# Optimization experiments

Hardware: AMD Instinct MI355X
Metric: run time of the kernel (lower is better)

The kernel has to match this reference:

```python
import jax, jax.numpy as jnp
import numpy as np

N = 50000
E = 800000
IN_CH = 128
HID = 128
HEADS = 2
NUM_GRAPHS = 1024
NEG_SLOPE = 0.2  # PyG GATConv default


def _gat_conv(x, src, dst, n, W, a_src, a_dst, b, heads, out_ch, concat):
    # x: [N, F_in]; src/dst: [E'] (self-loops already included)
    h = (x @ W).reshape(n, heads, out_ch)                # [N, H, C]
    alpha_src = jnp.sum(h * a_src, axis=-1)              # [N, H]
    alpha_dst = jnp.sum(h * a_dst, axis=-1)              # [N, H]
    e = alpha_src[src] + alpha_dst[dst]                  # [E', H]
    e = jnp.where(e > 0, e, NEG_SLOPE * e)               # leaky_relu
    # softmax over incoming edges of each destination node
    emax = jax.ops.segment_max(e, dst, num_segments=n)   # [N, H]
    ex = jnp.exp(e - emax[dst])
    denom = jax.ops.segment_sum(ex, dst, num_segments=n)
    alpha = ex / denom[dst]                              # [E', H]
    msg = h[src] * alpha[:, :, None]                     # [E', H, C]
    out = jax.ops.segment_sum(msg, dst, num_segments=n)  # [N, H, C]
    if concat:
        out = out.reshape(n, heads * out_ch)
    else:
        out = out.mean(axis=1)
    return out + b


def setup_inputs() -> dict:
    key = jax.random.key(0)
    ks = jax.random.split(key, 16)
    x = jax.random.normal(ks[0], (N, IN_CH), dtype=jnp.float32)
    edge_index = jax.random.randint(ks[1], (2, E), 0, N, dtype=jnp.int64)
    batch = jnp.sort(jax.random.randint(ks[2], (N,), 0, NUM_GRAPHS, dtype=jnp.int64))
    s = lambda fan_in: 1.0 / np.sqrt(fan_in)
    W1 = jax.random.normal(ks[3], (IN_CH, HEADS * HID), dtype=jnp.float32) * s(IN_CH)
    att_src1 = jax.random.normal(ks[4], (HEADS, HID), dtype=jnp.float32) * s(HID)
    att_dst1 = jax.random.normal(ks[5], (HEADS, HID), dtype=jnp.float32) * s(HID)
    b1 = jnp.zeros((HEADS * HID,), dtype=jnp.float32)
    W2 = jax.random.normal(ks[6], (HEADS * HID, HID), dtype=jnp.float32) * s(HEADS * HID)
    att_src2 = jax.random.normal(ks[7], (1, HID), dtype=jnp.float32) * s(HID)
    att_dst2 = jax.random.normal(ks[8], (1, HID), dtype=jnp.float32) * s(HID)
    b2 = jnp.zeros((HID,), dtype=jnp.float32)
    lw1 = jax.random.normal(ks[9], (HID, HID // 2), dtype=jnp.float32) * s(HID)
    lb1 = jnp.zeros((HID // 2,), dtype=jnp.float32)
    lw2 = jax.random.normal(ks[10], (HID // 2, 1), dtype=jnp.float32) * s(HID // 2)
    lb2 = jnp.zeros((1,), dtype=jnp.float32)
    return {"x": x, "edge_index": edge_index, "batch": batch, "num_graphs": NUM_GRAPHS,
            "W1": W1, "att_src1": att_src1, "att_dst1": att_dst1, "b1": b1,
            "W2": W2, "att_src2": att_src2, "att_dst2": att_dst2, "b2": b2,
            "lw1": lw1, "lb1": lb1, "lw2": lw2, "lb2": lb2}


def reference(x, edge_index, batch, num_graphs, W1, att_src1, att_dst1, b1, W2, att_src2, att_dst2, b2, lw1, lb1, lw2, lb2):
    n = x.shape[0]
    # PyG GATConv adds self-loops by default
    loops = jnp.arange(n, dtype=edge_index.dtype)
    src = jnp.concatenate([edge_index[0], loops])
    dst = jnp.concatenate([edge_index[1], loops])
    h = jax.nn.relu(_gat_conv(x, src, dst, n, W1, att_src1, att_dst1, b1, HEADS, HID, concat=True))
    h = jax.nn.relu(_gat_conv(h, src, dst, n, W2, att_src2, att_dst2, b2, 1, HID, concat=True))
    # global mean pool over batch index
    sums = jax.ops.segment_sum(h, batch, num_segments=num_graphs)        # [G, HID]
    cnt = jax.ops.segment_sum(jnp.ones((n,), h.dtype), batch, num_segments=num_graphs)
    pooled = sums / jnp.maximum(cnt, 1.0)[:, None]
    z = jax.nn.relu(pooled @ lw1 + lb1)
    return z @ lw2 + lb2                                                 # [G, 1]
```

## Files before the change

### kernel.cpp

```cpp
#include <hip/hip_runtime.h>

#define NN 50000
#define NE 800000
#define NEP (NN + NE)
#define NG 1024

__device__ inline unsigned short f2b(float f) {
    unsigned int u = __float_as_uint(f);
    unsigned int r = (u + 0x7FFFu + ((u >> 16) & 1u)) >> 16;
    return (unsigned short)r;
}
__device__ inline float b2f(unsigned short b) {
    return __uint_as_float(((unsigned int)b) << 16);
}

__global__ void detect_i64(const int* __restrict__ raw, int n32, int* __restrict__ flag)
{
    __shared__ int nz;
    int tid = threadIdx.x;
    if (tid == 0) nz = 0;
    __syncthreads();
    int cnt = 0;
    for (int i = tid; i < 1024; i += 256) {
        int p = n32 - 2048 + 2 * i + 1;
        if (p >= 0 && p < n32 && raw[p] != 0) cnt++;
    }
    atomicAdd(&nz, cnt);
    __syncthreads();
    if (tid == 0) flag[0] = (nz == 0) ? 1 : 0;
}

__global__ void cvt_idx(const int* __restrict__ raw, const int* __restrict__ flag,
                        int* __restrict__ out, int n)
{
    int i = blockIdx.x * 256 + threadIdx.x;
    if (i >= n) return;
    out[i] = flag[0] ? raw[2 * i] : raw[i];
}

__global__ void edge_hist(const int* __restrict__ ei, int* __restrict__ cnt)
{
    int e = blockIdx.x * 256 + threadIdx.x;
    if (e >= NEP) return;
    int dst = (e < NE) ? ei[NE + e] : (e - NE);
    atomicAdd(&cnt[dst], 1);
}

__global__ __launch_bounds__(1024) void scan_counts(const int* __restrict__ cnt,
                                                    int* __restrict__ rowptr, int n)
{
    __shared__ int wsums[16];
    __shared__ int carry_s;
    int tid = threadIdx.x, lane = tid & 63, wid = tid >> 6;
    if (tid == 0) carry_s = 0;
    __syncthreads();
    for (int base = 0; base < n; base += 1024) {
        int i = base + tid;
        int v = (i < n) ? cnt[i] : 0;
        int s = v;
        #pragma unroll
        for (int off = 1; off < 64; off <<= 1) {
            int t = __shfl_up(s, off);
            if (lane >= off) s += t;
        }
        if (lane == 63) wsums[wid] = s;
        __syncthreads();
        if (wid == 0 && lane < 16) {
            int ws = wsums[lane];
            #pragma unroll
            for (int off = 1; off < 16; off <<= 1) {
                int t = __shfl_up(ws, off);
                if (lane >= off) ws += t;
            }
            wsums[lane] = ws;
        }
        __syncthreads();
        int wave_off = (wid == 0) ? 0 : wsums[wid - 1];
        int carry = carry_s;
        if (i < n) rowptr[i] = carry + wave_off + s - v;
        int total = wsums[15];
        __syncthreads();
        if (tid == 0) carry_s = carry + total;
        __syncthreads();
    }
    if (tid == 0) rowptr[n] = carry_s;
}

__global__ void copy_int(const int* __restrict__ a, int* __restrict__ b, int n)
{
    int i = blockIdx.x * 256 + threadIdx.x;
    if (i < n) b[i] = a[i];
}

__global__ void edge_scatter(const int* __restrict__ ei, int* __restrict__ cursor,
                             int* __restrict__ csr_src)
{
    int e = blockIdx.x * 256 + threadIdx.x;
    if (e >= NEP) return;
    int src, dst;
    if (e < NE) { src = ei[e]; dst = ei[NE + e]; }
    else        { src = dst = e - NE; }
    int pos = atomicAdd(&cursor[dst], 1);
    csr_src[pos] = src;
}

template <int HEADS>
__global__ __launch_bounds__(256) void gemm_fused(const float* __restrict__ A,
                                                  const float* __restrict__ B,
                                                  unsigned short* __restrict__ Cb,
                                                  const float* __restrict__ att_src,
                                                  const float* __restrict__ att_dst,
                                                  float* __restrict__ asrc,
                                                  float* __restrict__ adst,
                                                  int M, int N, int K)
{
    const int BM = 128, BN = 128, BK = 16;
    __shared__ float As[BK][BM];
    __shared__ float Bs[BK][BN];
    int tid = threadIdx.x;
    int tx = tid & 15, ty = tid >> 4;
    int row0 = blockIdx.x * BM, col0 = blockIdx.y * BN;
    float acc[8][8] = {};
    for (int k0 = 0; k0 < K; k0 += BK) {
        #pragma unroll
        for (int i = 0; i < 2; i++) {
            int f4 = tid + i * 256;
            int r  = f4 >> 2;
            int c4 = (f4 & 3) << 2;
            float4 v = make_float4(0.f, 0.f, 0.f, 0.f);
            int gr = row0 + r;
            if (gr < M) v = *(const float4*)&A[(size_t)gr * K + k0 + c4];
            As[c4 + 0][r] = v.x; As[c4 + 1][r] = v.y;
            As[c4 + 2][r] = v.z; As[c4 + 3][r] = v.w;
        }
        #pragma unroll
        for (int i = 0; i < 2; i++) {
            int f4 = tid + i * 256;
            int r  = f4 >> 5;
            int c4 = (f4 & 31) << 2;
            *(float4*)&Bs[r][c4] = *(const float4*)&B[(size_t)(k0 + r) * N + col0 + c4];
        }
        __syncthreads();
        #pragma unroll
        for (int k = 0; k < BK; k++) {
            float av[8], bv[8];
            *(float4*)&av[0] = *(const float4*)&As[k][ty * 8];
            *(float4*)&av[4] = *(const float4*)&As[k][ty * 8 + 4];
            *(float4*)&bv[0] = *(const float4*)&Bs[k][tx * 8];
            *(float4*)&bv[4] = *(const float4*)&Bs[k][tx * 8 + 4];
            #pragma unroll
            for (int i = 0; i < 8; i++)
                #pragma unroll
                for (int j = 0; j < 8; j++)
                    acc[i][j] += av[i] * bv[j];
        }
        __syncthreads();
    }

    float vs[8], vd[8];
    #pragma unroll
    for (int j = 0; j < 8; j++) {
        vs[j] = att_src[col0 + tx * 8 + j];
        vd[j] = att_dst[col0 + tx * 8 + j];
    }
    int head = col0 >> 7;
    #pragma unroll
    for (int i = 0; i < 8; i++) {
        int gr = row0 + ty * 8 + i;
        if (gr < M) {
            float ps = 0.f, pd = 0.f;
            #pragma unroll
            for (int j = 0; j < 8; j++) { ps += acc[i][j] * vs[j]; pd += acc[i][j] * vd[j]; }
            #pragma unroll
            for (int off = 8; off > 0; off >>= 1) {
                ps += __shfl_xor(ps, off);
                pd += __shfl_xor(pd, off);
            }
            if (tx == 0) {
                atomicAdd(&asrc[gr * HEADS + head], ps);
                atomicAdd(&adst[gr * HEADS + head], pd);
            }
            #pragma unroll
            for (int j = 0; j < 8; j += 4) {
                ushort4 bvv;
                bvv.x = f2b(acc[i][j + 0]); bvv.y = f2b(acc[i][j + 1]);
                bvv.z = f2b(acc[i][j + 2]); bvv.w = f2b(acc[i][j + 3]);
                *(ushort4*)&Cb[(size_t)gr * N + col0 + tx * 8 + j] = bvv;
            }
        }
    }
}

template <int HEADS>
__global__ __launch_bounds__(256) void gat_aggregate(const unsigned short* __restrict__ hb,
                                                     const float* __restrict__ asrc,
                                                     const float* __restrict__ adst,
                                                     const int* __restrict__ rowptr,
                                                     const int* __restrict__ csr_src,
                                                     const float* __restrict__ bias,
                                                     float* __restrict__ out, int n)
{
    const int CH   = HEADS * 128;
    const int PER  = CH / 64;
    const int MAXE = 128;
    __shared__ float w_lds[4][MAXE * HEADS];
    __shared__ int   s_lds[4][MAXE];
    int wid = threadIdx.x >> 6, lane = threadIdx.x & 63;
    int node = blockIdx.x * 4 + wid;
    if (node >= n) return;

    int start = rowptr[node], end = rowptr[node + 1];
    int deg = end - start;
    bool fast = (deg <= MAXE);
    int head = (PER == 4) ? (lane >> 5) : 0;

    float ad[HEADS], m[HEADS], dsum[HEADS];
    #pragma unroll
    for (int hh = 0; hh < HEADS; hh++) { ad[hh] = adst[node * HEADS + hh]; m[hh] = -1e30f; dsum[hh] = 0.f; }

    for (int base = 0; base < deg; base += 64) {
        int j = base + lane;
        if (j < deg) {
            int s = csr_src[start + j];
            if (fast) s_lds[wid][j] = s;
            #pragma unroll
            for (int hh = 0; hh < HEADS; hh++) {
                float v = asrc[s * HEADS + hh] + ad[hh];
                v = (v > 0.f) ? v : 0.2f * v;
                if (fast) w_lds[wid][j * HEADS + hh] = v;
                m[hh] = fmaxf(m[hh], v);
            }
        }
    }
    #pragma unroll
    for (int hh = 0; hh < HEADS; hh++)
        #pragma unroll
        for (int off = 32; off > 0; off >>= 1)
            m[hh] = fmaxf(m[hh], __shfl_xor(m[hh], off));

    for (int base = 0; base < deg; base += 64) {
        int j = base + lane;
        if (j < deg) {
            #pragma unroll
            for (int hh = 0; hh < HEADS; hh++) {
                float v;
                if (fast) v = w_lds[wid][j * HEADS + hh];
                else {
                    int s = csr_src[start + j];
                    v = asrc[s * HEADS + hh] + ad[hh];
                    v = (v > 0.f) ? v : 0.2f * v;
                }
                float ex = __expf(v - m[hh]);
                if (fast) w_lds[wid][j * HEADS + hh] = ex;
                dsum[hh] += ex;
            }
        }
    }
    #pragma unroll
    for (int hh = 0; hh < HEADS; hh++)
        #pragma unroll
        for (int off = 32; off > 0; off >>= 1)
            dsum[hh] += __shfl_xor(dsum[hh], off);

    float m_l    = (HEADS == 2 && head) ? m[HEADS - 1] : m[0];
    float ad_l   = (HEADS == 2 && head) ? ad[HEADS - 1] : ad[0];
    float inv_l  = 1.0f / ((HEADS == 2 && head) ? dsum[HEADS - 1] : dsum[0]);

    float acc[PER];
    #pragma unroll
    for (int p = 0; p < PER; p++) acc[p] = 0.f;

    auto edge_sw = [&](int j, int& s, float& wgt) {
        if (fast) {
            s   = s_lds[wid][j];
            wgt = w_lds[wid][j * HEADS + head] * inv_l;
        } else {
            s = csr_src[start + j];
            float v = asrc[s * HEADS + head] + ad_l;
            v = (v > 0.f) ? v : 0.2f * v;
            wgt = __expf(v - m_l) * inv_l;
        }
    };

    const int U = 8;
    int j = 0;
    for (; j + U <= deg; j += U) {
        int su[U]; float wu[U];
        #pragma unroll
        for (int u = 0; u < U; u++) edge_sw(j + u, su[u], wu[u]);
        if (PER == 4) {
            ushort4 hv[U];
            #pragma unroll
            for (int u = 0; u < U; u++)
                hv[u] = *(const ushort4*)&hb[(size_t)su[u] * CH + lane * 4];
            #pragma unroll
            for (int u = 0; u < U; u++) {
                acc[0] += wu[u] * b2f(hv[u].x); acc[1] += wu[u] * b2f(hv[u].y);
                acc[2] += wu[u] * b2f(hv[u].z); acc[3] += wu[u] * b2f(hv[u].w);
            }
        } else {
            ushort2 hv[U];
            #pragma unroll
            for (int u = 0; u < U; u++)
                hv[u] = *(const ushort2*)&hb[(size_t)su[u] * CH + lane * 2];
            #pragma unroll
            for (int u = 0; u < U; u++) {
                acc[0] += wu[u] * b2f(hv[u].x); acc[1] += wu[u] * b2f(hv[u].y);
            }
        }
    }
    for (; j < deg; j++) {
        int s; float wgt;
        edge_sw(j, s, wgt);
        if (PER == 4) {
            ushort4 hv = *(const ushort4*)&hb[(size_t)s * CH + lane * 4];
            acc[0] += wgt * b2f(hv.x); acc[1] += wgt * b2f(hv.y);
            acc[2] += wgt * b2f(hv.z); acc[3] += wgt * b2f(hv.w);
        } else {
            ushort2 hv = *(const ushort2*)&hb[(size_t)s * CH + lane * 2];
            acc[0] += wgt * b2f(hv.x); acc[1] += wgt * b2f(hv.y);
        }
    }

    #pragma unroll
    for (int p = 0; p < PER; p++) {
        float v = acc[p] + bias[lane * PER + p];
        out[(size_t)node * CH + lane * PER + p] = fmaxf(v, 0.f);
    }
}

__global__ void find_bounds(const int* __restrict__ batch, int* __restrict__ bstart)
{
    int g = blockIdx.x * 256 + threadIdx.x;
    if (g > NG) return;
    if (g == NG) { bstart[NG] = NN; return; }
    int lo = 0, hi = NN;
    while (lo < hi) { int mid = (lo + hi) >> 1; if (batch[mid] < g) lo = mid + 1; else hi = mid; }
    bstart[g] = lo;
}

__global__ __launch_bounds__(256) void pool_seg(const float* __restrict__ h,
                                                const int* __restrict__ bstart,
                                                float* __restrict__ pooled)
{
    __shared__ float2 part[4][64];
    int g = blockIdx.x;
    int start = bstart[g], end = bstart[g + 1];
    int lane = threadIdx.x & 63, w = threadIdx.x >> 6;
    float2 acc = make_float2(0.f, 0.f);
    for (int i = start + w; i < end; i += 4) {
        float2 v = *(const float2*)&h[(size_t)i * 128 + lane * 2];
        acc.x += v.x; acc.y += v.y;
    }
    part[w][lane] = acc;
    __syncthreads();
    if (w == 0) {
        float2 s = part[0][lane];
        s.x += part[1][lane].x + part[2][lane].x + part[3][lane].x;
        s.y += part[1][lane].y + part[2][lane].y + part[3][lane].y;
        float invc = 1.0f / fmaxf((float)(end - start), 1.0f);
        pooled[g * 128 + lane * 2 + 0] = s.x * invc;
        pooled[g * 128 + lane * 2 + 1] = s.y * invc;
    }
}

__global__ __launch_bounds__(64) void head_mlp(const float* __restrict__ pooled,
                                               const float* __restrict__ lw1,
                                               const float* __restrict__ lb1,
                                               const float* __restrict__ lw2,
                                               const float* __restrict__ lb2,
                                               float* __restrict__ out)
{
    int g = blockIdx.x, lane = threadIdx.x;
    __shared__ float p[128];
    p[lane]      = pooled[g * 128 + lane];
    p[lane + 64] = pooled[g * 128 + lane + 64];
    __syncthreads();
    float z = lb1[lane];
    #pragma unroll 8
    for (int k = 0; k < 128; k++) z += p[k] * lw1[k * 64 + lane];
    z = fmaxf(z, 0.f);
    float v = z * lw2[lane];
    #pragma unroll
    for (int off = 32; off > 0; off >>= 1) v += __shfl_xor(v, off);
    if (lane == 0) out[g] = v + lb2[0];
}

extern "C" void kernel_launch(void* const* d_in, const int* in_sizes, int n_in,
                              void* d_out, int out_size, void* d_ws, size_t ws_size,
                              hipStream_t stream)
{
    const float* x      = (const float*)d_in[0];
    const int*   ei_raw = (const int*)d_in[1];
    const int*   bat_raw= (const int*)d_in[2];
    const float* W1   = (const float*)d_in[4];
    const float* as1  = (const float*)d_in[5];
    const float* ad1  = (const float*)d_in[6];
    const float* b1   = (const float*)d_in[7];
    const float* W2   = (const float*)d_in[8];
    const float* as2  = (const float*)d_in[9];
    const float* ad2  = (const float*)d_in[10];
    const float* b2   = (const float*)d_in[11];
    const float* lw1  = (const float*)d_in[12];
    const float* lb1  = (const float*)d_in[13];
    const float* lw2  = (const float*)d_in[14];
    const float* lb2  = (const float*)d_in[15];
    float* out = (float*)d_out;

    char* w = (char*)d_ws;
    auto alloc = [&](size_t bytes) { char* p = w; w += (bytes + 255) & ~size_t(255); return p; };
    float*          o1    = (float*)alloc((size_t)NN * 256 * 4);
    float*          o2    = (float*)alloc((size_t)NN * 128 * 4);
    unsigned short* h1b   = (unsigned short*)alloc((size_t)NN * 256 * 2);
    unsigned short* h2b   = (unsigned short*)alloc((size_t)NN * 128 * 2);
    float* alph  = (float*)alloc((size_t)NN * 6 * 4);
    float* asrc1 = alph;
    float* adst1 = alph + (size_t)NN * 2;
    float* asrc2 = alph + (size_t)NN * 4;
    float* adst2 = alph + (size_t)NN * 5;
    int*   cnts  = (int*)alloc((size_t)NN * 4);
    int*   rowp  = (int*)alloc((size_t)(NN + 4) * 4);
    int*   curs  = (int*)alloc((size_t)NN * 4);
    int*   csr   = (int*)alloc((size_t)NEP * 4);
    float* pooled= (float*)alloc((size_t)NG * 128 * 4);
    int*   bstart= (int*)alloc((size_t)(NG + 4) * 4);
    int*   ei32  = (int*)alloc((size_t)2 * NE * 4);
    int*   bat32 = (int*)alloc((size_t)NN * 4);
    int*   flags = (int*)alloc(2 * 4);

    detect_i64<<<1, 256, 0, stream>>>(ei_raw, 2 * NE, &flags[0]);
    detect_i64<<<1, 256, 0, stream>>>(bat_raw, NN, &flags[1]);
    cvt_idx<<<(2 * NE + 255) / 256, 256, 0, stream>>>(ei_raw, &flags[0], ei32, 2 * NE);
    cvt_idx<<<(NN + 255) / 256, 256, 0, stream>>>(bat_raw, &flags[1], bat32, NN);

    hipMemsetAsync(cnts, 0, NN * 4, stream);
    hipMemsetAsync(alph, 0, (size_t)NN * 6 * 4, stream);
    edge_hist<<<(NEP + 255) / 256, 256, 0, stream>>>(ei32, cnts);
    scan_counts<<<1, 1024, 0, stream>>>(cnts, rowp, NN);
    copy_int<<<(NN + 255) / 256, 256, 0, stream>>>(rowp, curs, NN);
    edge_scatter<<<(NEP + 255) / 256, 256, 0, stream>>>(ei32, curs, csr);

    gemm_fused<2><<<dim3((NN + 127) / 128, 2), 256, 0, stream>>>(
        x, W1, h1b, as1, ad1, asrc1, adst1, NN, 256, 128);
    gat_aggregate<2><<<(NN + 3) / 4, 256, 0, stream>>>(h1b, asrc1, adst1, rowp, csr, b1, o1, NN);

    gemm_fused<1><<<dim3((NN + 127) / 128, 1), 256, 0, stream>>>(
        o1, W2, h2b, as2, ad2, asrc2, adst2, NN, 128, 256);
    gat_aggregate<1><<<(NN + 3) / 4, 256, 0, stream>>>(h2b, asrc2, adst2, rowp, csr, b2, o2, NN);

    find_bounds<<<(NG + 1 + 255) / 256, 256, 0, stream>>>(bat32, bstart);
    pool_seg<<<NG, 256, 0, stream>>>(o2, bstart, pooled);
    head_mlp<<<NG, 64, 0, stream>>>(pooled, lw1, lb1, lw2, lb2, out);
}
```

Baseline: 491.7 us.

## Use bf16 MFMA GEMMs and fold index conversion and small kernels into consumers

```diff
diff --git a/kernel.cpp b/kernel.cpp
--- a/kernel.cpp
+++ b/kernel.cpp
@@ -4,6 +4,9 @@
 #define NE 800000
 #define NEP (NN + NE)
 #define NG 1024
+
+typedef short bf16x8 __attribute__((ext_vector_type(8)));
+typedef float f32x4  __attribute__((ext_vector_type(4)));
 
 __device__ inline unsigned short f2b(float f) {
     unsigned int u = __float_as_uint(f);
@@ -38,16 +41,19 @@
     out[i] = flag[0] ? raw[2 * i] : raw[i];
 }
 
-__global__ void edge_hist(const int* __restrict__ ei, int* __restrict__ cnt)
+__global__ void edge_hist(const int* __restrict__ raw, const int* __restrict__ flag,
+                          int* __restrict__ cnt)
 {
     int e = blockIdx.x * 256 + threadIdx.x;
     if (e >= NEP) return;
-    int dst = (e < NE) ? ei[NE + e] : (e - NE);
+    int f = flag[0];
+    int dst = (e < NE) ? (f ? raw[2 * (NE + e)] : raw[NE + e]) : (e - NE);
     atomicAdd(&cnt[dst], 1);
 }
 
 __global__ __launch_bounds__(1024) void scan_counts(const int* __restrict__ cnt,
-                                                    int* __restrict__ rowptr, int n)
+                                                    int* __restrict__ rowptr,
+                                                    int* __restrict__ curs, int n)
 {
     __shared__ int wsums[16];
     __shared__ int carry_s;
@@ -77,7 +83,11 @@
         __syncthreads();
         int wave_off = (wid == 0) ? 0 : wsums[wid - 1];
         int carry = carry_s;
-        if (i < n) rowptr[i] = carry + wave_off + s - v;
+        if (i < n) {
+            int ex = carry + wave_off + s - v;
+            rowptr[i] = ex;
+            curs[i]   = ex;
+        }
         int total = wsums[15];
         __syncthreads();
         if (tid == 0) carry_s = carry + total;
@@ -86,106 +96,119 @@
     if (tid == 0) rowptr[n] = carry_s;
 }
 
-__global__ void copy_int(const int* __restrict__ a, int* __restrict__ b, int n)
-{
-    int i = blockIdx.x * 256 + threadIdx.x;
-    if (i < n) b[i] = a[i];
-}
-
-__global__ void edge_scatter(const int* __restrict__ ei, int* __restrict__ cursor,
-                             int* __restrict__ csr_src)
+__global__ void edge_scatter(const int* __restrict__ raw, const int* __restrict__ flag,
+                             int* __restrict__ cursor, int* __restrict__ csr_src)
 {
     int e = blockIdx.x * 256 + threadIdx.x;
     if (e >= NEP) return;
+    int f = flag[0];
     int src, dst;
-    if (e < NE) { src = ei[e]; dst = ei[NE + e]; }
-    else        { src = dst = e - NE; }
+    if (e < NE) {
+        src = f ? raw[2 * e] : raw[e];
+        dst = f ? raw[2 * (NE + e)] : raw[NE + e];
+    } else { src = dst = e - NE; }
     int pos = atomicAdd(&cursor[dst], 1);
     csr_src[pos] = src;
 }
 
+__global__ void cast_bf16_vec(const float* __restrict__ in, unsigned short* __restrict__ out,
+                              int n4)
+{
+    int i = blockIdx.x * 256 + threadIdx.x;
+    if (i >= n4) return;
+    float4 v = ((const float4*)in)[i];
+    ushort4 o;
+    o.x = f2b(v.x); o.y = f2b(v.y); o.z = f2b(v.z); o.w = f2b(v.w);
+    ((ushort4*)out)[i] = o;
+}
+
+__global__ void cast_transpose(const float* __restrict__ W, unsigned short* __restrict__ Wt,
+                               int K, int N)
+{
+    int idx = blockIdx.x * 256 + threadIdx.x;
+    if (idx >= K * N) return;
+    int n = idx / K, k = idx - n * K;
+    Wt[idx] = f2b(W[(size_t)k * N + n]);
+}
+
 template <int HEADS>
-__global__ __launch_bounds__(256) void gemm_fused(const float* __restrict__ A,
-                                                  const float* __restrict__ B,
-                                                  unsigned short* __restrict__ Cb,
-                                                  const float* __restrict__ att_src,
-                                                  const float* __restrict__ att_dst,
-                                                  float* __restrict__ asrc,
-                                                  float* __restrict__ adst,
-                                                  int M, int N, int K)
-{
-    const int BM = 128, BN = 128, BK = 16;
-    __shared__ float As[BK][BM];
-    __shared__ float Bs[BK][BN];
-    int tid = threadIdx.x;
-    int tx = tid & 15, ty = tid >> 4;
-    int row0 = blockIdx.x * BM, col0 = blockIdx.y * BN;
-    float acc[8][8] = {};
+__global__ __launch_bounds__(256) void gemm_mfma(const unsigned short* __restrict__ A,
+                                                 const unsigned short* __restrict__ Bt,
+                                                 unsigned short* __restrict__ Cb,
+                                                 const float* __restrict__ att_src,
+                                                 const float* __restrict__ att_dst,
+                                                 float* __restrict__ asrc,
+                                                 float* __restrict__ adst,
+                                                 int M, int N, int K)
+{
+    const int BM = 128, BK = 32, LDT = 40;
+    __shared__ unsigned short As[BM * LDT];
+    __shared__ unsigned short Bs[BM * LDT];
+    int tid = threadIdx.x, lane = tid & 63, wid = tid >> 6;
+    int wm = wid >> 1, wn = wid & 1;
+    int row0 = blockIdx.x * BM, col0 = blockIdx.y * 128;
+    f32x4 acc[4][4] = {};
+
     for (int k0 = 0; k0 < K; k0 += BK) {
         #pragma unroll
         for (int i = 0; i < 2; i++) {
-            int f4 = tid + i * 256;
-            int r  = f4 >> 2;
-            int c4 = (f4 & 3) << 2;
-            float4 v = make_float4(0.f, 0.f, 0.f, 0.f);
-            int gr = row0 + r;
-            if (gr < M) v = *(const float4*)&A[(size_t)gr * K + k0 + c4];
-            As[c4 + 0][r] = v.x; As[c4 + 1][r] = v.y;
-            As[c4 + 2][r] = v.z; As[c4 + 3][r] = v.w;
-        }
-        #pragma unroll
-        for (int i = 0; i < 2; i++) {
-            int f4 = tid + i * 256;
-            int r  = f4 >> 5;
-            int c4 = (f4 & 31) << 2;
-            *(float4*)&Bs[r][c4] = *(const float4*)&B[(size_t)(k0 + r) * N + col0 + c4];
-        }
-        __syncthreads();
-        #pragma unroll
-        for (int k = 0; k < BK; k++) {
-            float av[8], bv[8];
-            *(float4*)&av[0] = *(const float4*)&As[k][ty * 8];
-            *(float4*)&av[4] = *(const float4*)&As[k][ty * 8 + 4];
-            *(float4*)&bv[0] = *(const float4*)&Bs[k][tx * 8];
-            *(float4*)&bv[4] = *(const float4*)&Bs[k][tx * 8 + 4];
-            #pragma unroll
-            for (int i = 0; i < 8; i++)
+            int id = tid + i * 256;
+            int r = id >> 2, c8 = (id & 3) * 8;
+            int4 va = make_int4(0, 0, 0, 0);
+            if (row0 + r < M)
+                va = *(const int4*)&A[(size_t)(row0 + r) * K + k0 + c8];
+            *(int4*)&As[r * LDT + c8] = va;
+            int4 vb = *(const int4*)&Bt[(size_t)(col0 + r) * K + k0 + c8];
+            *(int4*)&Bs[r * LDT + c8] = vb;
+        }
+        __syncthreads();
+        bf16x8 a[4], b[4];
+        #pragma unroll
+        for (int mr = 0; mr < 4; mr++)
+            a[mr] = *(const bf16x8*)&As[(wm * 64 + mr * 16 + (lane & 15)) * LDT + (lane >> 4) * 8];
+        #pragma unroll
+        for (int nr = 0; nr < 4; nr++)
+            b[nr] = *(const bf16x8*)&Bs[(wn * 64 + nr * 16 + (lane & 15)) * LDT + (lane >> 4) * 8];
+        #pragma unroll
+        for (int mr = 0; mr < 4; mr++)
+            #pragma unroll
+            for (int nr = 0; nr < 4; nr++)
+                acc[mr][nr] = __builtin_amdgcn_mfma_f32_16x16x32_bf16(a[mr], b[nr], acc[mr][nr], 0, 0, 0);
+        __syncthreads();
+    }
+
+    int colbase = col0 + wn * 64;
+    int head = colbase >> 7;
+    float vs[4], vd[4];
+    #pragma unroll
+    for (int nr = 0; nr < 4; nr++) {
+        vs[nr] = att_src[colbase + nr * 16 + (lane & 15)];
+        vd[nr] = att_dst[colbase + nr * 16 + (lane & 15)];
+    }
+    #pragma unroll
+    for (int mr = 0; mr < 4; mr++) {
+        #pragma unroll
+        for (int r = 0; r < 4; r++) {
+            int row = row0 + wm * 64 + mr * 16 + (lane >> 4) * 4 + r;
+            if (row < M) {
+                float ps = 0.f, pd = 0.f;
                 #pragma unroll
-                for (int j = 0; j < 8; j++)
-                    acc[i][j] += av[i] * bv[j];
-        }
-        __syncthreads();
-    }
-
-    float vs[8], vd[8];
-    #pragma unroll
-    for (int j = 0; j < 8; j++) {
-        vs[j] = att_src[col0 + tx * 8 + j];
-        vd[j] = att_dst[col0 + tx * 8 + j];
-    }
-    int head = col0 >> 7;
-    #pragma unroll
-    for (int i = 0; i < 8; i++) {
-        int gr = row0 + ty * 8 + i;
-        if (gr < M) {
-            float ps = 0.f, pd = 0.f;
-            #pragma unroll
-            for (int j = 0; j < 8; j++) { ps += acc[i][j] * vs[j]; pd += acc[i][j] * vd[j]; }
-            #pragma unroll
-            for (int off = 8; off > 0; off >>= 1) {
-                ps += __shfl_xor(ps, off);
-                pd += __shfl_xor(pd, off);
-            }
-            if (tx == 0) {
-                atomicAdd(&asrc[gr * HEADS + head], ps);
-                atomicAdd(&adst[gr * HEADS + head], pd);
-            }
-            #pragma unroll
-            for (int j = 0; j < 8; j += 4) {
-                ushort4 bvv;
-                bvv.x = f2b(acc[i][j + 0]); bvv.y = f2b(acc[i][j + 1]);
-                bvv.z = f2b(acc[i][j + 2]); bvv.w = f2b(acc[i][j + 3]);
-                *(ushort4*)&Cb[(size_t)gr * N + col0 + tx * 8 + j] = bvv;
+                for (int nr = 0; nr < 4; nr++) {
+                    ps += acc[mr][nr][r] * vs[nr];
+                    pd += acc[mr][nr][r] * vd[nr];
+                }
+                #pragma unroll
+                for (int off = 8; off > 0; off >>= 1) {
+                    ps += __shfl_xor(ps, off);
+                    pd += __shfl_xor(pd, off);
+                }
+                if ((lane & 15) == 0) {
+                    atomicAdd(&asrc[row * HEADS + head], ps);
+                    atomicAdd(&adst[row * HEADS + head], pd);
+                }
+                #pragma unroll
+                for (int nr = 0; nr < 4; nr++)
+                    Cb[(size_t)row * N + colbase + nr * 16 + (lane & 15)] = f2b(acc[mr][nr][r]);
             }
         }
     }
@@ -198,7 +221,8 @@
                                                      const int* __restrict__ rowptr,
                                                      const int* __restrict__ csr_src,
                                                      const float* __restrict__ bias,
-                                                     float* __restrict__ out, int n)
+                                                     unsigned short* __restrict__ outb,
+                                                     float* __restrict__ outf, int n)
 {
     const int CH   = HEADS * 128;
     const int PER  = CH / 64;
@@ -322,30 +346,33 @@
         }
     }
 
-    #pragma unroll
-    for (int p = 0; p < PER; p++) {
-        float v = acc[p] + bias[lane * PER + p];
-        out[(size_t)node * CH + lane * PER + p] = fmaxf(v, 0.f);
-    }
-}
-
-__global__ void find_bounds(const int* __restrict__ batch, int* __restrict__ bstart)
-{
-    int g = blockIdx.x * 256 + threadIdx.x;
-    if (g > NG) return;
-    if (g == NG) { bstart[NG] = NN; return; }
+    if (HEADS == 2) {
+        ushort4 ov;
+        ov.x = f2b(fmaxf(acc[0] + bias[lane * 4 + 0], 0.f));
+        ov.y = f2b(fmaxf(acc[1] + bias[lane * 4 + 1], 0.f));
+        ov.z = f2b(fmaxf(acc[2] + bias[lane * 4 + 2], 0.f));
+        ov.w = f2b(fmaxf(acc[3] + bias[lane * 4 + 3], 0.f));
+        *(ushort4*)&outb[(size_t)node * 256 + lane * 4] = ov;
+    } else {
+        float2 ov;
+        ov.x = fmaxf(acc[0] + bias[lane * 2 + 0], 0.f);
+        ov.y = fmaxf(acc[1] + bias[lane * 2 + 1], 0.f);
+        *(float2*)&outf[(size_t)node * 128 + lane * 2] = ov;
+    }
+}
+
+__global__ __launch_bounds__(256) void pool_seg(const float* __restrict__ h,
+                                                const int* __restrict__ batch,
+                                                float* __restrict__ pooled)
+{
+    __shared__ float2 part[4][64];
+    int g = blockIdx.x;
     int lo = 0, hi = NN;
     while (lo < hi) { int mid = (lo + hi) >> 1; if (batch[mid] < g) lo = mid + 1; else hi = mid; }
-    bstart[g] = lo;
-}
-
-__global__ __launch_bounds__(256) void pool_seg(const float* __restrict__ h,
-                                                const int* __restrict__ bstart,
-                                                float* __restrict__ pooled)
-{
-    __shared__ float2 part[4][64];
-    int g = blockIdx.x;
-    int start = bstart[g], end = bstart[g + 1];
+    int start = lo;
+    lo = 0; hi = NN;
+    while (lo < hi) { int mid = (lo + hi) >> 1; if (batch[mid] < g + 1) lo = mid + 1; else hi = mid; }
+    int end = lo;
     int lane = threadIdx.x & 63, w = threadIdx.x >> 6;
     float2 acc = make_float2(0.f, 0.f);
     for (int i = start + w; i < end; i += 4) {
@@ -409,10 +436,13 @@
 
     char* w = (char*)d_ws;
     auto alloc = [&](size_t bytes) { char* p = w; w += (bytes + 255) & ~size_t(255); return p; };
-    float*          o1    = (float*)alloc((size_t)NN * 256 * 4);
-    float*          o2    = (float*)alloc((size_t)NN * 128 * 4);
+    unsigned short* xb    = (unsigned short*)alloc((size_t)NN * 128 * 2);
+    unsigned short* w1t   = (unsigned short*)alloc((size_t)256 * 128 * 2);
+    unsigned short* w2t   = (unsigned short*)alloc((size_t)128 * 256 * 2);
     unsigned short* h1b   = (unsigned short*)alloc((size_t)NN * 256 * 2);
     unsigned short* h2b   = (unsigned short*)alloc((size_t)NN * 128 * 2);
+    unsigned short* o1b   = (unsigned short*)alloc((size_t)NN * 256 * 2);
+    float*          o2    = (float*)alloc((size_t)NN * 128 * 4);
     float* alph  = (float*)alloc((size_t)NN * 6 * 4);
     float* asrc1 = alph;
     float* adst1 = alph + (size_t)NN * 2;
@@ -423,32 +453,33 @@
     int*   curs  = (int*)alloc((size_t)NN * 4);
     int*   csr   = (int*)alloc((size_t)NEP * 4);
     float* pooled= (float*)alloc((size_t)NG * 128 * 4);
-    int*   bstart= (int*)alloc((size_t)(NG + 4) * 4);
-    int*   ei32  = (int*)alloc((size_t)2 * NE * 4);
     int*   bat32 = (int*)alloc((size_t)NN * 4);
     int*   flags = (int*)alloc(2 * 4);
 
     detect_i64<<<1, 256, 0, stream>>>(ei_raw, 2 * NE, &flags[0]);
     detect_i64<<<1, 256, 0, stream>>>(bat_raw, NN, &flags[1]);
-    cvt_idx<<<(2 * NE + 255) / 256, 256, 0, stream>>>(ei_raw, &flags[0], ei32, 2 * NE);
     cvt_idx<<<(NN + 255) / 256, 256, 0, stream>>>(bat_raw, &flags[1], bat32, NN);
 
     hipMemsetAsync(cnts, 0, NN * 4, stream);
     hipMemsetAsync(alph, 0, (size_t)NN * 6 * 4, stream);
-    edge_hist<<<(NEP + 255) / 256, 256, 0, stream>>>(ei32, cnts);
-    scan_counts<<<1, 1024, 0, stream>>>(cnts, rowp, NN);
-    copy_int<<<(NN + 255) / 256, 256, 0, stream>>>(rowp, curs, NN);
-    edge_scatter<<<(NEP + 255) / 256, 256, 0, stream>>>(ei32, curs, csr);
-
-    gemm_fused<2><<<dim3((NN + 127) / 128, 2), 256, 0, stream>>>(
-        x, W1, h1b, as1, ad1, asrc1, adst1, NN, 256, 128);
-    gat_aggregate<2><<<(NN + 3) / 4, 256, 0, stream>>>(h1b, asrc1, adst1, rowp, csr, b1, o1, NN);
-
-    gemm_fused<1><<<dim3((NN + 127) / 128, 1), 256, 0, stream>>>(
-        o1, W2, h2b, as2, ad2, asrc2, adst2, NN, 128, 256);
-    gat_aggregate<1><<<(NN + 3) / 4, 256, 0, stream>>>(h2b, asrc2, adst2, rowp, csr, b2, o2, NN);
-
-    find_bounds<<<(NG + 1 + 255) / 256, 256, 0, stream>>>(bat32, bstart);
-    pool_seg<<<NG, 256, 0, stream>>>(o2, bstart, pooled);
+    edge_hist<<<(NEP + 255) / 256, 256, 0, stream>>>(ei_raw, &flags[0], cnts);
+    scan_counts<<<1, 1024, 0, stream>>>(cnts, rowp, curs, NN);
+    edge_scatter<<<(NEP + 255) / 256, 256, 0, stream>>>(ei_raw, &flags[0], curs, csr);
+
+    cast_bf16_vec<<<(NN * 128 / 4 + 255) / 256, 256, 0, stream>>>(x, xb, NN * 128 / 4);
+    cast_transpose<<<(256 * 128 + 255) / 256, 256, 0, stream>>>(W1, w1t, 128, 256);
+    cast_transpose<<<(128 * 256 + 255) / 256, 256, 0, stream>>>(W2, w2t, 256, 128);
+
+    gemm_mfma<2><<<dim3((NN + 127) / 128, 2), 256, 0, stream>>>(
+        xb, w1t, h1b, as1, ad1, asrc1, adst1, NN, 256, 128);
+    gat_aggregate<2><<<(NN + 3) / 4, 256, 0, stream>>>(h1b, asrc1, adst1, rowp, csr, b1,
+                                                       o1b, nullptr, NN);
+
+    gemm_mfma<1><<<dim3((NN + 127) / 128, 1), 256, 0, stream>>>(
+        o1b, w2t, h2b, as2, ad2, asrc2, adst2, NN, 128, 256);
+    gat_aggregate<1><<<(NN + 3) / 4, 256, 0, stream>>>(h2b, asrc2, adst2, rowp, csr, b2,
+                                                       nullptr, o2, NN);
+
+    pool_seg<<<NG, 256, 0, stream>>>(o2, bat32, pooled);
     head_mlp<<<NG, 64, 0, stream>>>(pooled, lw1, lb1, lw2, lb2, out);
 }
```

Result: faster. 435.7 us (-11.4%).
